# Optimization experiments

Hardware: AMD Instinct MI355X
Metric: run time of the kernel (lower is better)

The kernel has to match this reference:

```python
import jax, jax.numpy as jnp
import numpy as np

B, DIM, H, W = 64, 384, 28, 28
NH, HD, WS, SS = 6, 64, 7, 3
HID = 1536
N = WS * WS
NW = (H // WS) * (W // WS)
SCALE = HD ** -0.25  # qk_scale=None -> head_dim ** -0.25, applied to both q and k
EPS = 1e-5


def _rel_pos_index(ws):
    coords = np.stack(np.meshgrid(np.arange(ws), np.arange(ws), indexing='ij'))  # (2,ws,ws)
    flat = coords.reshape(2, -1)
    rel = (flat[:, :, None] - flat[:, None, :]).transpose(1, 2, 0).copy()  # (N,N,2)
    rel[..., 0] += ws - 1
    rel[..., 1] += ws - 1
    rel[..., 0] *= 2 * ws - 1
    return rel.sum(-1)  # (N,N) int


def _attn_mask(h, w, ws, ss):
    img = np.zeros((h, w))
    cnt = 0
    for hs in (slice(0, -ws), slice(-ws, -ss), slice(-ss, None)):
        for wsl in (slice(0, -ws), slice(-ws, -ss), slice(-ss, None)):
            img[hs, wsl] = cnt
            cnt += 1
    mw = img.reshape(h // ws, ws, w // ws, ws).transpose(0, 2, 1, 3).reshape(-1, ws * ws)  # (nW,N)
    diff = mw[:, None, :] - mw[:, :, None]
    return np.where(diff != 0, -100.0, 0.0).astype(np.float32)  # (nW,N,N)


REL_IDX = jnp.asarray(_rel_pos_index(WS))          # (N,N)
MASK = jnp.asarray(_attn_mask(H, W, WS, SS))       # (NW,N,N)


def _layernorm_bchw(x, w, b):
    mean = jnp.mean(x, axis=1, keepdims=True)
    var = jnp.var(x, axis=1, keepdims=True, ddof=1)  # torch.var_mean is unbiased
    return (x - mean) / jnp.sqrt(var + EPS) * w + b


def setup_inputs() -> dict:
    key = jax.random.key(0)
    ks = jax.random.split(key, 6)
    return {
        'x': jax.random.normal(ks[0], (B, DIM, H, W), jnp.float32),
        'norm1_w': jnp.ones((1, DIM, 1, 1), jnp.float32),
        'norm1_b': jnp.zeros((1, DIM, 1, 1), jnp.float32),
        'qkv_w': jax.random.normal(ks[1], (3 * NH * HD, DIM), jnp.float32) * 0.02,
        'rel_bias_table': jax.random.normal(ks[2], ((2 * WS - 1) ** 2, NH), jnp.float32) * 0.02,
        'proj_w': jax.random.normal(ks[3], (DIM, NH * HD), jnp.float32) * 0.02,
        'norm2_w': jnp.ones((1, DIM, 1, 1), jnp.float32),
        'norm2_b': jnp.zeros((1, DIM, 1, 1), jnp.float32),
        'mlp_w1': jax.random.normal(ks[4], (HID, DIM), jnp.float32) * 0.02,
        'mlp_w3': jax.random.normal(ks[5], (DIM, HID), jnp.float32) * 0.02,
    }


def reference(x, norm1_w, norm1_b, qkv_w, rel_bias_table, proj_w, norm2_w, norm2_b, mlp_w1, mlp_w3):
    b = x.shape[0]
    shortcut = x
    xn = _layernorm_bchw(x, norm1_w, norm1_b)
    xs = jnp.roll(xn, (-SS, -SS), axis=(2, 3))
    # window partition: (B,C,H,W) -> (B*nW, C, WS, WS)
    xw = xs.reshape(b, DIM, H // WS, WS, W // WS, WS).transpose(0, 2, 4, 1, 3, 5).reshape(-1, DIM, WS, WS)
    bw = xw.shape[0]
    # 1x1-conv qkv projection (no bias), then split heads
    qkv = jnp.einsum('oc,bchw->bohw', qkv_w, xw).reshape(bw, 3, NH, HD, N)
    q, k, v = jnp.moveaxis(qkv, 1, 0)  # each (bw, NH, HD, N)
    attn = jnp.einsum('bhdn,bhdm->bhnm', q * SCALE, k * SCALE)  # (bw,NH,N,N)
    bias = rel_bias_table[REL_IDX.reshape(-1)].reshape(N, N, NH).transpose(2, 0, 1)  # (NH,N,N)
    attn = attn + bias[None]
    attn = attn.reshape(b, NW, NH, N, N) + MASK[None, :, None]
    attn = jax.nn.softmax(attn.reshape(bw, NH, N, N), axis=-1)
    out = jnp.einsum('bhnm,bhdm->bhdn', attn, v)  # (bw,NH,HD,N)
    out = out.reshape(bw, NH * HD, WS, WS)
    out = jnp.einsum('oc,bchw->bohw', proj_w, out)
    # window reverse + unshift
    xr = out.reshape(b, H // WS, W // WS, DIM, WS, WS).transpose(0, 3, 1, 4, 2, 5).reshape(b, DIM, H, W)
    xr = jnp.roll(xr, (SS, SS), axis=(2, 3))
    x = shortcut + xr
    # conv MLP (1x1 convs, no bias, exact GELU)
    xn2 = _layernorm_bchw(x, norm2_w, norm2_b)
    h = jax.nn.gelu(jnp.einsum('oc,bchw->bohw', mlp_w1, xn2), approximate=False)
    x = x + jnp.einsum('oc,bchw->bohw', mlp_w3, h)
    return x
```

## Files before the change

kernel.cpp:

```cpp
#include <hip/hip_runtime.h>
#include <hip/hip_bf16.h>


typedef __bf16 bf16x8 __attribute__((ext_vector_type(8)));
typedef __bf16 bf16x4 __attribute__((ext_vector_type(4)));
typedef float  f32x4  __attribute__((ext_vector_type(4)));

#define GAS __attribute__((address_space(1)))
#define LAS __attribute__((address_space(3)))

__device__ __forceinline__ void gload_lds16(const void* g, void* l) {
  __builtin_amdgcn_global_load_lds((const GAS void*)g, (LAS void*)l, 16, 0, 0);
}

__device__ __forceinline__ int div7u(int m) { return (m * 37) >> 8; }

__device__ __forceinline__ float gelu_f(float v) {
  float s = fabsf(v) * 0.70710678118f;
  float t = __builtin_amdgcn_rcpf(__builtin_fmaf(0.3275911f, s, 1.f));
  float p = t * (0.254829592f +
            t * (-0.284496736f +
            t * (1.421413741f +
            t * (-1.453152027f +
            t * 1.061405429f))));
  float erfa = __builtin_fmaf(-p, __expf(-s * s), 1.f);
  return __builtin_fmaf(0.5f * fabsf(v), erfa, 0.5f * v);
}

__global__ __launch_bounds__(256) void cvt_all_kernel(const float* __restrict__ s0,
                                                      const float* __restrict__ s1,
                                                      const float* __restrict__ s2,
                                                      const float* __restrict__ s3,
                                                      __bf16* __restrict__ d0,
                                                      __bf16* __restrict__ d1,
                                                      __bf16* __restrict__ d2,
                                                      __bf16* __restrict__ d3) {
  int i = blockIdx.x * 256 + threadIdx.x;
  if (i < 442368) { d0[i] = (__bf16)s0[i]; return; }
  i -= 442368;
  if (i < 147456) { d1[i] = (__bf16)s1[i]; return; }
  i -= 147456;
  if (i < 589824) { d2[i] = (__bf16)s2[i]; return; }
  i -= 589824;
  d3[i] = (__bf16)s3[i];
}

__global__ __launch_bounds__(256) void bias_expand_kernel(const float* __restrict__ tbl,
                                                          float* __restrict__ be) {
  int idx = blockIdx.x * 256 + threadIdx.x;
  if (idx >= 6 * 64 * 64) return;
  int m = idx & 63, n = (idx >> 6) & 63, h = idx >> 12;
  float v = 0.f;
  if (m < 49 && n < 49) {
    int in_ = div7u(n), jn = n - in_ * 7;
    int im  = div7u(m), jm = m - im * 7;
    int t = (in_ - im + 6) * 13 + (jn - jm + 6);
    v = tbl[t * 6 + h];
  }
  be[idx] = v;
}

__global__ __launch_bounds__(256) void ln_t_kernel(const float* __restrict__ x,
                                                   const float* __restrict__ gw,
                                                   const float* __restrict__ gb,
                                                   __bf16* __restrict__ out) {
  __shared__ f32x4 ps[16][16], ps2[16][16];
  __shared__ __align__(16) __bf16 tile[64][198];
  const int tid = threadIdx.x;
  const int lane = tid & 63, w = tid >> 6;
  const int gq = lane & 15;
  const int sub = (w << 2) + (lane >> 4);
  const int tok0 = blockIdx.x << 6;
  const int tokg4 = tok0 + (gq << 2);
  const unsigned b = (unsigned)tokg4 / 784u;
  const unsigned p = (unsigned)tokg4 - b * 784u;
  const float* xp = x + (size_t)b * 301056u + p;

  f32x4 vals[24];
  f32x4 s4 = {0.f, 0.f, 0.f, 0.f}, s24 = {0.f, 0.f, 0.f, 0.f};
  #pragma unroll
  for (int half = 0; half < 2; ++half)
    #pragma unroll
    for (int k = 0; k < 12; ++k) {
      int c = half * 192 + sub * 12 + k;
      f32x4 v = *(const f32x4*)(xp + (size_t)c * 784u);
      vals[half * 12 + k] = v;
      s4 += v;
      s24 += v * v;
    }
  ps[sub][gq] = s4;
  ps2[sub][gq] = s24;
  __syncthreads();
  f32x4 S = {0.f, 0.f, 0.f, 0.f}, S2 = {0.f, 0.f, 0.f, 0.f};
  #pragma unroll
  for (int i = 0; i < 16; ++i) { S += ps[i][gq]; S2 += ps2[i][gq]; }
  f32x4 mean = S * (1.f / 384.f);
  f32x4 var = (S2 - S * mean) * (1.f / 383.f);
  f32x4 rstd;
  #pragma unroll
  for (int j = 0; j < 4; ++j) rstd[j] = rsqrtf(var[j] + 1e-5f);

  #pragma unroll
  for (int half = 0; half < 2; ++half) {
    if (half) __syncthreads();
    #pragma unroll
    for (int k = 0; k < 12; ++k) {
      int c = half * 192 + sub * 12 + k;
      float wgt = gw[c], bia = gb[c];
      f32x4 v = (vals[half * 12 + k] - mean) * rstd * wgt + bia;
      #pragma unroll
      for (int j = 0; j < 4; ++j)
        tile[(gq << 2) + j][sub * 12 + k] = (__bf16)v[j];
    }
    __syncthreads();
    #pragma unroll
    for (int it = 0; it < 6; ++it) {
      int idx = (it << 8) + tid;
      int row = idx / 24, colc = idx - row * 24;
      bf16x8 vv = *(const bf16x8*)(&tile[row][colc << 3]);
      *(bf16x8*)(out + (size_t)(tok0 + row) * 384 + half * 192 + (colc << 3)) = vv;
    }
  }
}

template <int EPI>
__global__ __launch_bounds__(256, 2) void gemm_bt(const __bf16* __restrict__ A, int lda,
                                                  const __bf16* __restrict__ Bt, int ldb,
                                                  int K, int My,
                                                  __bf16* __restrict__ outT, int ldo, int ocol,
                                                  float* __restrict__ outR,
                                                  const float* __restrict__ resid,
                                                  int tok_off) {
  __shared__ __align__(16) char smem[65536];
  const int tid = threadIdx.x;
  const int lane = tid & 63;
  const int w = tid >> 6;
  const int wr = w >> 1, wc = w & 1;
  const int c = lane & 15, g = lane >> 4;

  const int nwg = gridDim.x;
  const int orig = blockIdx.x;
  const int q = nwg >> 3, r = nwg & 7;
  const int xcd = orig & 7, ii = orig >> 3;
  const int base = xcd < r ? xcd * (q + 1) : r * (q + 1) + (xcd - r) * q;
  const int wgid = base + ii;
  const int bx = wgid / My;
  const int by = wgid - bx * My;
  const int m0 = by << 7;
  const int n0 = bx << 7;

  const __bf16* ap[4];
  const __bf16* bp[4];
  #pragma unroll
  for (int i = 0; i < 4; ++i) {
    int s = (i << 8) + tid;
    int row = s >> 3;
    int kk = ((s ^ row) & 7) << 3;
    ap[i] = A  + (size_t)(m0 + row) * lda + kk;
    bp[i] = Bt + (size_t)(n0 + row) * ldb + kk;
  }
  auto stage = [&](int buf, int k0) {
    #pragma unroll
    for (int i = 0; i < 4; ++i) {
      gload_lds16(ap[i] + k0, smem + (buf << 15) + (((i << 8) + (w << 6)) << 4));
      gload_lds16(bp[i] + k0, smem + (buf << 15) + 16384 + (((i << 8) + (w << 6)) << 4));
    }
  };

  f32x4 acc[4][4] = {};
  const int nt = K >> 6;
  stage(0, 0);
  int cur = 0;
  for (int t = 0; t < nt; ++t) {
    if (t + 1 < nt) {
      stage(cur ^ 1, (t + 1) << 6);
      asm volatile("s_waitcnt vmcnt(8)" ::: "memory");
    } else {
      asm volatile("s_waitcnt vmcnt(0)" ::: "memory");
    }
    __builtin_amdgcn_s_barrier();
    __builtin_amdgcn_sched_barrier(0);
    const char* smA = smem + (cur << 15);
    const char* smB = smA + 16384;
    #pragma unroll
    for (int ks = 0; ks < 2; ++ks) {
      bf16x8 af[4], bfv[4];
      #pragma unroll
      for (int mi = 0; mi < 4; ++mi) {
        int r2 = (wr << 6) + (mi << 4) + c;
        af[mi] = *(const bf16x8*)(smA + (r2 << 7) + (((ks << 6) + (g << 4)) ^ ((r2 & 7) << 4)));
      }
      #pragma unroll
      for (int nj = 0; nj < 4; ++nj) {
        int r2 = (wc << 6) + (nj << 4) + c;
        bfv[nj] = *(const bf16x8*)(smB + (r2 << 7) + (((ks << 6) + (g << 4)) ^ ((r2 & 7) << 4)));
      }
      #pragma unroll
      for (int mi = 0; mi < 4; ++mi)
        #pragma unroll
        for (int nj = 0; nj < 4; ++nj) {
          if constexpr (EPI == 2)
            acc[mi][nj] = __builtin_amdgcn_mfma_f32_16x16x32_bf16(bfv[nj], af[mi], acc[mi][nj], 0, 0, 0);
          else
            acc[mi][nj] = __builtin_amdgcn_mfma_f32_16x16x32_bf16(af[mi], bfv[nj], acc[mi][nj], 0, 0, 0);
        }
    }
    __builtin_amdgcn_s_barrier();
    cur ^= 1;
  }

  if constexpr (EPI <= 1) {
    #pragma unroll
    for (int mi = 0; mi < 4; ++mi)
      #pragma unroll
      for (int nj = 0; nj < 4; ++nj) {
        f32x4 v = acc[mi][nj];
        if constexpr (EPI == 1) {
          #pragma unroll
          for (int r2 = 0; r2 < 4; ++r2) v[r2] = gelu_f(v[r2]);
        }
        bf16x4 pk = {(__bf16)v[0], (__bf16)v[1], (__bf16)v[2], (__bf16)v[3]};
        int nl = (wc << 6) + (nj << 4) + c;
        int ml = (wr << 6) + (mi << 4) + (g << 2);
        *(bf16x4*)(smem + nl * 264 + ml * 2) = pk;
      }
    __syncthreads();
    #pragma unroll
    for (int it = 0; it < 8; ++it) {
      int id = (it << 8) + tid;
      int n = id >> 4, mc = id & 15;
      bf16x8 v = *(const bf16x8*)(smem + n * 264 + (mc << 4));
      *(bf16x8*)(outT + (size_t)(n0 + n) * ldo + (ocol + m0 + (mc << 3))) = v;
    }
  } else {
    #pragma unroll
    for (int nj = 0; nj < 4; ++nj) {
      int tokb = tok_off + n0 + (wc << 6) + (nj << 4) + (g << 2);
      unsigned bb = (unsigned)tokb / 784u;
      unsigned pp = (unsigned)tokb - bb * 784u;
      size_t base2 = (size_t)bb * (384u * 784u) + pp;
      #pragma unroll
      for (int mi = 0; mi < 4; ++mi) {
        int o = m0 + (wr << 6) + (mi << 4) + c;
        size_t a2 = base2 + (size_t)o * 784u;
        f32x4 rv = *(const f32x4*)(resid + a2);
        f32x4 v = acc[mi][nj] + rv;
        *(f32x4*)(outR + a2) = v;
      }
    }
  }
}

__global__ __launch_bounds__(256, 2) void attn_kernel(const __bf16* __restrict__ qkv,
                                                      const float* __restrict__ be,
                                                      __bf16* __restrict__ outt) {
  __shared__ __align__(16) char smem_all[4][16384];
  const int tid = threadIdx.x;
  const int lane = tid & 63;
  const int w = tid >> 6;
  char* sm = (char*)smem_all[w];
  const int pair = blockIdx.x * 4 + w;
  const int h = pair % 6;
  const int wg = pair / 6;
  const int b = wg >> 4;
  const int wi = wg & 15;
  const int wh = wi >> 2, wwi = wi & 3;
  const int cc = lane & 15, g = lane >> 4;

  {
    int rsub = lane >> 3;
    int slot = lane & 7;
    int dc = (slot ^ rsub) << 3;
    #pragma unroll
    for (int i = 0; i < 8; ++i) {
      int r = i * 8 + rsub;
      int m = r < 49 ? r : 48;
      int im = div7u(m), jm = m - im * 7;
      int sh = wh * 7 + im + 3; if (sh >= 28) sh -= 28;
      int sw = wwi * 7 + jm + 3; if (sw >= 28) sw -= 28;
      size_t trow = (size_t)(b * 784 + sh * 28 + sw) * 1152;
      gload_lds16(qkv + trow + 384 + h * 64 + dc, sm + i * 1024);
      gload_lds16(qkv + trow +       h * 64 + dc, sm + 8192 + i * 1024);
    }
  }
  asm volatile("s_waitcnt vmcnt(0)" ::: "memory");
  __syncthreads();

  f32x4 sacc[4][4] = {};
  #pragma unroll
  for (int ks = 0; ks < 2; ++ks) {
    bf16x8 kf[4], qf[4];
    #pragma unroll
    for (int mi = 0; mi < 4; ++mi) {
      int r = (mi << 4) + cc;
      kf[mi] = *(const bf16x8*)(sm + (r << 7) + (((ks << 6) + (g << 4)) ^ ((r & 7) << 4)));
    }
    #pragma unroll
    for (int nj = 0; nj < 4; ++nj) {
      int r = (nj << 4) + cc;
      qf[nj] = *(const bf16x8*)(sm + 8192 + (r << 7) + (((ks << 6) + (g << 4)) ^ ((r & 7) << 4)));
    }
    #pragma unroll
    for (int mi = 0; mi < 4; ++mi)
      #pragma unroll
      for (int nj = 0; nj < 4; ++nj)
        sacc[mi][nj] = __builtin_amdgcn_mfma_f32_16x16x32_bf16(kf[mi], qf[nj], sacc[mi][nj], 0, 0, 0);
  }
  __syncthreads();

  int r9m[4][4];
  #pragma unroll
  for (int mi = 0; mi < 4; ++mi)
    #pragma unroll
    for (int rr = 0; rr < 4; ++rr) {
      int m = (mi << 4) + (g << 2) + rr; if (m > 48) m = 48;
      int im = div7u(m), jm = m - im * 7;
      int sh = wh * 7 + im, sw = wwi * 7 + jm;
      r9m[mi][rr] = ((sh < 21) ? 0 : (sh < 25 ? 1 : 2)) * 3 + ((sw < 21) ? 0 : (sw < 25 ? 1 : 2));
    }

  #pragma unroll
  for (int nj = 0; nj < 4; ++nj) {
    int n = (nj << 4) + cc;
    int ncl = n > 48 ? 48 : n;
    int in_ = div7u(ncl), jn = ncl - in_ * 7;
    int shn = wh * 7 + in_, swn = wwi * 7 + jn;
    int r9n = ((shn < 21) ? 0 : (shn < 25 ? 1 : 2)) * 3 + ((swn < 21) ? 0 : (swn < 25 ? 1 : 2));
    float mx = -1e30f;
    #pragma unroll
    for (int mi = 0; mi < 4; ++mi) {
      f32x4 bia = *(const f32x4*)(be + (((h << 6) + n) << 6) + (mi << 4) + (g << 2));
      #pragma unroll
      for (int rr = 0; rr < 4; ++rr) {
        int m = (mi << 4) + (g << 2) + rr;
        float t = (m < 49)
            ? sacc[mi][nj][rr] * 0.125f + bia[rr] + ((r9m[mi][rr] == r9n) ? 0.f : -100.f)
            : -1e30f;
        sacc[mi][nj][rr] = t;
        mx = fmaxf(mx, t);
      }
    }
    mx = fmaxf(mx, __shfl_xor(mx, 16, 64));
    mx = fmaxf(mx, __shfl_xor(mx, 32, 64));
    float sum = 0.f;
    #pragma unroll
    for (int mi = 0; mi < 4; ++mi)
      #pragma unroll
      for (int rr = 0; rr < 4; ++rr) {
        float e = __expf(sacc[mi][nj][rr] - mx);
        sacc[mi][nj][rr] = e;
        sum += e;
      }
    sum += __shfl_xor(sum, 16, 64);
    sum += __shfl_xor(sum, 32, 64);
    float inv = __builtin_amdgcn_rcpf(sum);
    #pragma unroll
    for (int mi = 0; mi < 4; ++mi) {
      bf16x4 pk = {(__bf16)(sacc[mi][nj][0] * inv), (__bf16)(sacc[mi][nj][1] * inv),
                   (__bf16)(sacc[mi][nj][2] * inv), (__bf16)(sacc[mi][nj][3] * inv)};
      *(bf16x4*)(sm + 8192 + (n << 7) + (((mi << 5) + (g << 3)) ^ ((n & 7) << 4))) = pk;
    }
  }

  {
    int ml = lane & 15, dq = lane >> 4;
    #pragma unroll
    for (int it = 0; it < 4; ++it) {
      int m = (it << 4) + ml;
      int mc_ = m > 48 ? 48 : m;
      int im = div7u(mc_), jm = mc_ - im * 7;
      int sh = wh * 7 + im + 3; if (sh >= 28) sh -= 28;
      int sw = wwi * 7 + jm + 3; if (sw >= 28) sw -= 28;
      const __bf16* gv = qkv + (size_t)(b * 784 + sh * 28 + sw) * 1152 + 768 + h * 64;
      #pragma unroll
      for (int hd = 0; hd < 2; ++hd) {
        int dbase = (hd << 5) + (dq << 3);
        bf16x8 v = *(const bf16x8*)(gv + dbase);
        #pragma unroll
        for (int j = 0; j < 8; ++j) {
          int d = dbase + j;
          *(__bf16*)(sm + (d << 7) + ((((m >> 3) ^ (d & 7)) << 4) + ((m & 7) << 1))) = v[j];
        }
      }
    }
  }
  __syncthreads();

  f32x4 oacc[4][4] = {};
  #pragma unroll
  for (int ks = 0; ks < 2; ++ks) {
    bf16x8 pf[4], vf[4];
    #pragma unroll
    for (int ni = 0; ni < 4; ++ni) {
      int n = (ni << 4) + cc;
      pf[ni] = *(const bf16x8*)(sm + 8192 + (n << 7) + (((ks << 6) + (g << 4)) ^ ((n & 7) << 4)));
    }
    #pragma unroll
    for (int dj = 0; dj < 4; ++dj) {
      int d = (dj << 4) + cc;
      vf[dj] = *(const bf16x8*)(sm + (d << 7) + ((((ks << 2) + g) ^ (d & 7)) << 4));
    }
    #pragma unroll
    for (int ni = 0; ni < 4; ++ni)
      #pragma unroll
      for (int dj = 0; dj < 4; ++dj)
        oacc[ni][dj] = __builtin_amdgcn_mfma_f32_16x16x32_bf16(pf[ni], vf[dj], oacc[ni][dj], 0, 0, 0);
  }

  #pragma unroll
  for (int ni = 0; ni < 4; ++ni)
    #pragma unroll
    for (int rr = 0; rr < 4; ++rr) {
      int n = (ni << 4) + (g << 2) + rr;
      if (n < 49) {
        int im = div7u(n), jn = n - im * 7;
        int sh = wh * 7 + im + 3; if (sh >= 28) sh -= 28;
        int sw = wwi * 7 + jn + 3; if (sw >= 28) sw -= 28;
        __bf16* op = outt + (size_t)(b * 784 + sh * 28 + sw) * 384 + h * 64;
        #pragma unroll
        for (int dj = 0; dj < 4; ++dj)
          op[(dj << 4) + cc] = (__bf16)oacc[ni][dj][rr];
      }
    }
}

extern "C" void kernel_launch(void* const* d_in, const int* in_sizes, int n_in,
                              void* d_out, int out_size, void* d_ws, size_t ws_size,
                              hipStream_t stream) {
  (void)in_sizes; (void)n_in; (void)out_size; (void)ws_size;
  const float* x     = (const float*)d_in[0];
  const float* n1w   = (const float*)d_in[1];
  const float* n1b   = (const float*)d_in[2];
  const float* qkvw  = (const float*)d_in[3];
  const float* tbl   = (const float*)d_in[4];
  const float* projw = (const float*)d_in[5];
  const float* n2w   = (const float*)d_in[6];
  const float* n2b   = (const float*)d_in[7];
  const float* w1    = (const float*)d_in[8];
  const float* w3    = (const float*)d_in[9];
  float* out = (float*)d_out;

  char* ws = (char*)d_ws;
  __bf16* bufA = (__bf16*)ws;
  __bf16* bufB = (__bf16*)(ws + 38535168);
  float*  be   = (float*)(ws + 154140672);
  __bf16* wq   = (__bf16*)(ws + 154238976);
  __bf16* wp   = wq + 442368;
  __bf16* wm1  = wp + 147456;
  __bf16* wm3  = wm1 + 589824;

  cvt_all_kernel<<<6912, 256, 0, stream>>>(qkvw, projw, w1, w3, wq, wp, wm1, wm3);
  bias_expand_kernel<<<96, 256, 0, stream>>>(tbl, be);

  ln_t_kernel<<<784, 256, 0, stream>>>(x, n1w, n1b, bufA);
  gemm_bt<0><<<392 * 9, 256, 0, stream>>>(wq, 384, bufA, 384, 384, 9, bufB, 1152, 0,
                                          nullptr, nullptr, 0);
  attn_kernel<<<1536, 256, 0, stream>>>(bufB, be, bufA);
  gemm_bt<2><<<392 * 3, 256, 0, stream>>>(wp, 384, bufA, 384, 384, 3, nullptr, 0, 0,
                                          out, x, 0);
  ln_t_kernel<<<784, 256, 0, stream>>>(out, n2w, n2b, bufA);
  for (int hh = 0; hh < 2; ++hh) {
    const int toff = hh * 25088;
    gemm_bt<1><<<196 * 12, 256, 0, stream>>>(wm1, 384, bufA + (size_t)toff * 384, 384, 384, 12,
                                             bufB, 1536, 0, nullptr, nullptr, 0);
    gemm_bt<2><<<196 * 3, 256, 0, stream>>>(wm3, 1536, bufB, 1536, 1536, 3,
                                            nullptr, 0, 0, out, out, toff);
  }
}
```

Before: 399.1 us.

## Add 256x256-tile 8-wave GEMM for QKV and MLP-up projections

Adds a new gemm256 kernel with 256x256 output tiles, 512 threads, K fixed at 384, staged double buffering interleaved with MFMA phases and s_setprio hints. It replaces the 128x128 gemm_bt for the QKV projection (M padded from 1152 to 1280 with clamped loads and a masked store) and the MLP first layer with GELU. The larger tile raises arithmetic intensity and cuts global and LDS traffic per FLOP. In exchange it uses 128KB of LDS and many accumulator registers, which limits occupancy, and wastes compute on the padded M rows for QKV. gemm_bt is reduced to the residual-add epilogue only.

```diff
diff --git a/kernel.cpp b/kernel.cpp
--- a/kernel.cpp
+++ b/kernel.cpp
@@ -124,10 +124,160 @@
 }
 
 template <int EPI>
+__global__ __launch_bounds__(512, 2) void gemm256(const __bf16* __restrict__ A,
+                                                  const __bf16* __restrict__ Bt, int ldb,
+                                                  int My, int Mreal,
+                                                  __bf16* __restrict__ outT, int ldo) {
+  __shared__ __align__(16) char smem[131072];
+  const int tid = threadIdx.x;
+  const int lane = tid & 63;
+  const int w = tid >> 6;
+  const int wr = w >> 2, wc = w & 3;
+  const int c = lane & 15, g = lane >> 4;
+
+  const int nwg = gridDim.x;
+  const int orig = blockIdx.x;
+  const int q = nwg >> 3, r = nwg & 7;
+  const int xcd = orig & 7, ii = orig >> 3;
+  const int wgid = (xcd < r ? xcd * (q + 1) : r * (q + 1) + (xcd - r) * q) + ii;
+  const int bx = wgid / My;
+  const int by = wgid - bx * My;
+  const int m0 = by << 8;
+  const int n0 = bx << 8;
+
+  const int r0 = tid >> 3;
+  const int kk = ((tid & 7) ^ ((tid >> 3) & 7)) << 3;
+  const __bf16* pA[4];
+  const __bf16* pB[4];
+  #pragma unroll
+  for (int j = 0; j < 4; ++j) {
+    int ra = m0 + j * 64 + r0; if (ra > Mreal - 1) ra = Mreal - 1;
+    pA[j] = A + (size_t)ra * 384 + kk;
+    pB[j] = Bt + (size_t)(n0 + j * 64 + r0) * ldb + kk;
+  }
+  const int dstw = w << 10;
+  auto stage = [&](int buf, int ht, int k0) {
+    char* d = smem + (buf << 16) + (ht << 14) + dstw;
+    const __bf16* p0 = (ht < 2) ? pA[ht << 1] : pB[(ht - 2) << 1];
+    const __bf16* p1 = (ht < 2) ? pA[(ht << 1) + 1] : pB[((ht - 2) << 1) + 1];
+    gload_lds16(p0 + k0, d);
+    gload_lds16(p1 + k0, d + 8192);
+  };
+
+  const int off0 = (g << 4) ^ ((c & 7) << 4);
+  const int off1 = off0 ^ 64;
+  const int aB = (wr << 14) + (c << 7);
+  const int bB = 32768 + (wc << 13) + (c << 7);
+
+  f32x4 acc[8][4];
+  #pragma unroll
+  for (int i = 0; i < 8; ++i)
+    #pragma unroll
+    for (int j = 0; j < 4; ++j) acc[i][j] = (f32x4){0.f, 0.f, 0.f, 0.f};
+
+  stage(0, 0, 0); stage(0, 1, 0); stage(0, 2, 0); stage(0, 3, 0);
+
+  bf16x8 aX[4], aY[4], b0[4], b1[4];
+  #pragma unroll
+  for (int t = 0; t < 6; ++t) {
+    const int cur = t & 1, nxt = cur ^ 1;
+    const int k1 = (t + 1) << 6;
+    const char* sc = smem + (cur << 16);
+    __builtin_amdgcn_s_barrier();
+    if (t < 5) {
+      stage(nxt, 0, k1);
+      asm volatile("s_waitcnt vmcnt(2)" ::: "memory");
+    } else {
+      asm volatile("s_waitcnt vmcnt(0)" ::: "memory");
+    }
+    __builtin_amdgcn_s_barrier();
+    #pragma unroll
+    for (int mi = 0; mi < 4; ++mi) aX[mi] = *(const bf16x8*)(sc + aB + mi * 2048 + off0);
+    #pragma unroll
+    for (int nj = 0; nj < 4; ++nj) b0[nj] = *(const bf16x8*)(sc + bB + nj * 2048 + off0);
+    asm volatile("s_waitcnt lgkmcnt(0)" ::: "memory");
+    __builtin_amdgcn_sched_barrier(0);
+    __builtin_amdgcn_s_setprio(1);
+    #pragma unroll
+    for (int mi = 0; mi < 4; ++mi)
+      #pragma unroll
+      for (int nj = 0; nj < 4; ++nj)
+        acc[mi][nj] = __builtin_amdgcn_mfma_f32_16x16x32_bf16(aX[mi], b0[nj], acc[mi][nj], 0, 0, 0);
+    __builtin_amdgcn_s_setprio(0);
+    #pragma unroll
+    for (int mi = 0; mi < 4; ++mi) aY[mi] = *(const bf16x8*)(sc + aB + (4 + mi) * 2048 + off0);
+    if (t < 5) stage(nxt, 1, k1);
+    asm volatile("s_waitcnt lgkmcnt(0)" ::: "memory");
+    __builtin_amdgcn_sched_barrier(0);
+    __builtin_amdgcn_s_setprio(1);
+    #pragma unroll
+    for (int mi = 0; mi < 4; ++mi)
+      #pragma unroll
+      for (int nj = 0; nj < 4; ++nj)
+        acc[4 + mi][nj] = __builtin_amdgcn_mfma_f32_16x16x32_bf16(aY[mi], b0[nj], acc[4 + mi][nj], 0, 0, 0);
+    __builtin_amdgcn_s_setprio(0);
+    #pragma unroll
+    for (int mi = 0; mi < 4; ++mi) aX[mi] = *(const bf16x8*)(sc + aB + mi * 2048 + off1);
+    #pragma unroll
+    for (int nj = 0; nj < 4; ++nj) b1[nj] = *(const bf16x8*)(sc + bB + nj * 2048 + off1);
+    if (t < 5) stage(nxt, 2, k1);
+    asm volatile("s_waitcnt lgkmcnt(0)" ::: "memory");
+    __builtin_amdgcn_sched_barrier(0);
+    __builtin_amdgcn_s_setprio(1);
+    #pragma unroll
+    for (int mi = 0; mi < 4; ++mi)
+      #pragma unroll
+      for (int nj = 0; nj < 4; ++nj)
+        acc[mi][nj] = __builtin_amdgcn_mfma_f32_16x16x32_bf16(aX[mi], b1[nj], acc[mi][nj], 0, 0, 0);
+    __builtin_amdgcn_s_setprio(0);
+    #pragma unroll
+    for (int mi = 0; mi < 4; ++mi) aY[mi] = *(const bf16x8*)(sc + aB + (4 + mi) * 2048 + off1);
+    if (t < 5) stage(nxt, 3, k1);
+    asm volatile("s_waitcnt lgkmcnt(0)" ::: "memory");
+    __builtin_amdgcn_sched_barrier(0);
+    __builtin_amdgcn_s_setprio(1);
+    #pragma unroll
+    for (int mi = 0; mi < 4; ++mi)
+      #pragma unroll
+      for (int nj = 0; nj < 4; ++nj)
+        acc[4 + mi][nj] = __builtin_amdgcn_mfma_f32_16x16x32_bf16(aY[mi], b1[nj], acc[4 + mi][nj], 0, 0, 0);
+    __builtin_amdgcn_s_setprio(0);
+  }
+
+  __syncthreads();
+  char* tw = smem + (w << 14);
+  #pragma unroll
+  for (int mi = 0; mi < 8; ++mi)
+    #pragma unroll
+    for (int nj = 0; nj < 4; ++nj) {
+      f32x4 v = acc[mi][nj];
+      if constexpr (EPI == 1) {
+        #pragma unroll
+        for (int j = 0; j < 4; ++j) v[j] = gelu_f(v[j]);
+      }
+      bf16x4 pk = {(__bf16)v[0], (__bf16)v[1], (__bf16)v[2], (__bf16)v[3]};
+      int tok = (nj << 4) + c;
+      int mb = (mi << 5) + (g << 3);
+      *(bf16x4*)(tw + (tok << 8) + (mb ^ ((tok & 7) << 4))) = pk;
+    }
+  __syncthreads();
+  const int tokl = lane >> 4;
+  const int ch = lane & 15;
+  const int mg = m0 + (wr << 7) + (ch << 3);
+  if (mg < Mreal) {
+    #pragma unroll
+    for (int rep = 0; rep < 16; ++rep) {
+      int tok = (rep << 2) + tokl;
+      bf16x8 v = *(const bf16x8*)(tw + (tok << 8) + ((ch << 4) ^ ((tok & 7) << 4)));
+      *(bf16x8*)(outT + (size_t)(n0 + (wc << 6) + tok) * ldo + mg) = v;
+    }
+  }
+}
+
+template <int EPI>
 __global__ __launch_bounds__(256, 2) void gemm_bt(const __bf16* __restrict__ A, int lda,
                                                   const __bf16* __restrict__ Bt, int ldb,
                                                   int K, int My,
-                                                  __bf16* __restrict__ outT, int ldo, int ocol,
                                                   float* __restrict__ outR,
                                                   const float* __restrict__ resid,
                                                   int tok_off) {
@@ -155,9 +305,9 @@
   for (int i = 0; i < 4; ++i) {
     int s = (i << 8) + tid;
     int row = s >> 3;
-    int kk = ((s ^ row) & 7) << 3;
-    ap[i] = A  + (size_t)(m0 + row) * lda + kk;
-    bp[i] = Bt + (size_t)(n0 + row) * ldb + kk;
+    int kkk = ((s ^ row) & 7) << 3;
+    ap[i] = A  + (size_t)(m0 + row) * lda + kkk;
+    bp[i] = Bt + (size_t)(n0 + row) * ldb + kkk;
   }
   auto stage = [&](int buf, int k0) {
     #pragma unroll
@@ -198,55 +348,26 @@
       #pragma unroll
       for (int mi = 0; mi < 4; ++mi)
         #pragma unroll
-        for (int nj = 0; nj < 4; ++nj) {
-          if constexpr (EPI == 2)
-            acc[mi][nj] = __builtin_amdgcn_mfma_f32_16x16x32_bf16(bfv[nj], af[mi], acc[mi][nj], 0, 0, 0);
-          else
-            acc[mi][nj] = __builtin_amdgcn_mfma_f32_16x16x32_bf16(af[mi], bfv[nj], acc[mi][nj], 0, 0, 0);
-        }
+        for (int nj = 0; nj < 4; ++nj)
+          acc[mi][nj] = __builtin_amdgcn_mfma_f32_16x16x32_bf16(bfv[nj], af[mi], acc[mi][nj], 0, 0, 0);
     }
     __builtin_amdgcn_s_barrier();
     cur ^= 1;
   }
 
-  if constexpr (EPI <= 1) {
-    #pragma unroll
-    for (int mi = 0; mi < 4; ++mi)
-      #pragma unroll
-      for (int nj = 0; nj < 4; ++nj) {
-        f32x4 v = acc[mi][nj];
-        if constexpr (EPI == 1) {
-          #pragma unroll
-          for (int r2 = 0; r2 < 4; ++r2) v[r2] = gelu_f(v[r2]);
-        }
-        bf16x4 pk = {(__bf16)v[0], (__bf16)v[1], (__bf16)v[2], (__bf16)v[3]};
-        int nl = (wc << 6) + (nj << 4) + c;
-        int ml = (wr << 6) + (mi << 4) + (g << 2);
-        *(bf16x4*)(smem + nl * 264 + ml * 2) = pk;
-      }
-    __syncthreads();
-    #pragma unroll
-    for (int it = 0; it < 8; ++it) {
-      int id = (it << 8) + tid;
-      int n = id >> 4, mc = id & 15;
-      bf16x8 v = *(const bf16x8*)(smem + n * 264 + (mc << 4));
-      *(bf16x8*)(outT + (size_t)(n0 + n) * ldo + (ocol + m0 + (mc << 3))) = v;
-    }
-  } else {
-    #pragma unroll
-    for (int nj = 0; nj < 4; ++nj) {
-      int tokb = tok_off + n0 + (wc << 6) + (nj << 4) + (g << 2);
-      unsigned bb = (unsigned)tokb / 784u;
-      unsigned pp = (unsigned)tokb - bb * 784u;
-      size_t base2 = (size_t)bb * (384u * 784u) + pp;
-      #pragma unroll
-      for (int mi = 0; mi < 4; ++mi) {
-        int o = m0 + (wr << 6) + (mi << 4) + c;
-        size_t a2 = base2 + (size_t)o * 784u;
-        f32x4 rv = *(const f32x4*)(resid + a2);
-        f32x4 v = acc[mi][nj] + rv;
-        *(f32x4*)(outR + a2) = v;
-      }
+  #pragma unroll
+  for (int nj = 0; nj < 4; ++nj) {
+    int tokb = tok_off + n0 + (wc << 6) + (nj << 4) + (g << 2);
+    unsigned bb = (unsigned)tokb / 784u;
+    unsigned pp = (unsigned)tokb - bb * 784u;
+    size_t base2 = (size_t)bb * (384u * 784u) + pp;
+    #pragma unroll
+    for (int mi = 0; mi < 4; ++mi) {
+      int o = m0 + (wr << 6) + (mi << 4) + c;
+      size_t a2 = base2 + (size_t)o * 784u;
+      f32x4 rv = *(const f32x4*)(resid + a2);
+      f32x4 v = acc[mi][nj] + rv;
+      *(f32x4*)(outR + a2) = v;
     }
   }
 }
@@ -453,17 +574,15 @@
   bias_expand_kernel<<<96, 256, 0, stream>>>(tbl, be);
 
   ln_t_kernel<<<784, 256, 0, stream>>>(x, n1w, n1b, bufA);
-  gemm_bt<0><<<392 * 9, 256, 0, stream>>>(wq, 384, bufA, 384, 384, 9, bufB, 1152, 0,
-                                          nullptr, nullptr, 0);
+  gemm256<0><<<196 * 5, 512, 0, stream>>>(wq, bufA, 384, 5, 1152, bufB, 1152);
   attn_kernel<<<1536, 256, 0, stream>>>(bufB, be, bufA);
-  gemm_bt<2><<<392 * 3, 256, 0, stream>>>(wp, 384, bufA, 384, 384, 3, nullptr, 0, 0,
-                                          out, x, 0);
+  gemm_bt<2><<<392 * 3, 256, 0, stream>>>(wp, 384, bufA, 384, 384, 3, out, x, 0);
   ln_t_kernel<<<784, 256, 0, stream>>>(out, n2w, n2b, bufA);
   for (int hh = 0; hh < 2; ++hh) {
     const int toff = hh * 25088;
-    gemm_bt<1><<<196 * 12, 256, 0, stream>>>(wm1, 384, bufA + (size_t)toff * 384, 384, 384, 12,
-                                             bufB, 1536, 0, nullptr, nullptr, 0);
+    gemm256<1><<<98 * 6, 512, 0, stream>>>(wm1, bufA + (size_t)toff * 384, 384, 6, 1536,
+                                           bufB, 1536);
     gemm_bt<2><<<196 * 3, 256, 0, stream>>>(wm3, 1536, bufB, 1536, 1536, 3,
-                                            nullptr, 0, 0, out, out, toff);
-  }
-}
+                                            out, out, toff);
+  }
+}
```

Result: slower. 419.6 us (+5.1%).

## Replace double-buffered direct-to-LDS GEMM loads with register-staged single buffer

Applied to the files above, without the earlier changes.

The GEMM kernel stops using global_load_lds into two LDS buffers. It now prefetches the next K tile into registers during the MFMA loop and writes it to a single LDS buffer between two barriers. This halves LDS use, which allows launch bounds of three workgroups per CU for higher occupancy. In exchange it adds VGPR pressure, register-to-LDS store traffic and an extra barrier per iteration, and the global load latency is only hidden within a single compute phase.

```diff
diff --git a/kernel.cpp b/kernel.cpp
--- a/kernel.cpp
+++ b/kernel.cpp
@@ -5,13 +5,10 @@
 typedef __bf16 bf16x8 __attribute__((ext_vector_type(8)));
 typedef __bf16 bf16x4 __attribute__((ext_vector_type(4)));
 typedef float  f32x4  __attribute__((ext_vector_type(4)));
+typedef int    i32x4  __attribute__((ext_vector_type(4)));
 
 #define GAS __attribute__((address_space(1)))
 #define LAS __attribute__((address_space(3)))
-
-__device__ __forceinline__ void gload_lds16(const void* g, void* l) {
-  __builtin_amdgcn_global_load_lds((const GAS void*)g, (LAS void*)l, 16, 0, 0);
-}
 
 __device__ __forceinline__ int div7u(int m) { return (m * 37) >> 8; }
 
@@ -124,14 +121,14 @@
 }
 
 template <int EPI>
-__global__ __launch_bounds__(256, 2) void gemm_bt(const __bf16* __restrict__ A, int lda,
+__global__ __launch_bounds__(256, 3) void gemm_bt(const __bf16* __restrict__ A, int lda,
                                                   const __bf16* __restrict__ Bt, int ldb,
                                                   int K, int My,
                                                   __bf16* __restrict__ outT, int ldo, int ocol,
                                                   float* __restrict__ outR,
                                                   const float* __restrict__ resid,
                                                   int tok_off) {
-  __shared__ __align__(16) char smem[65536];
+  __shared__ __align__(16) char smem[33792];
   const int tid = threadIdx.x;
   const int lane = tid & 63;
   const int w = tid >> 6;
@@ -142,8 +139,7 @@
   const int orig = blockIdx.x;
   const int q = nwg >> 3, r = nwg & 7;
   const int xcd = orig & 7, ii = orig >> 3;
-  const int base = xcd < r ? xcd * (q + 1) : r * (q + 1) + (xcd - r) * q;
-  const int wgid = base + ii;
+  const int wgid = (xcd < r ? xcd * (q + 1) : r * (q + 1) + (xcd - r) * q) + ii;
   const int bx = wgid / My;
   const int by = wgid - bx * My;
   const int m0 = by << 7;
@@ -159,29 +155,38 @@
     ap[i] = A  + (size_t)(m0 + row) * lda + kk;
     bp[i] = Bt + (size_t)(n0 + row) * ldb + kk;
   }
-  auto stage = [&](int buf, int k0) {
-    #pragma unroll
-    for (int i = 0; i < 4; ++i) {
-      gload_lds16(ap[i] + k0, smem + (buf << 15) + (((i << 8) + (w << 6)) << 4));
-      gload_lds16(bp[i] + k0, smem + (buf << 15) + 16384 + (((i << 8) + (w << 6)) << 4));
-    }
+
+  i32x4 sA0, sA1, sA2, sA3, sB0, sB1, sB2, sB3;
+  auto issue = [&](int k0) {
+    sA0 = *(const i32x4*)(ap[0] + k0); sB0 = *(const i32x4*)(bp[0] + k0);
+    sA1 = *(const i32x4*)(ap[1] + k0); sB1 = *(const i32x4*)(bp[1] + k0);
+    sA2 = *(const i32x4*)(ap[2] + k0); sB2 = *(const i32x4*)(bp[2] + k0);
+    sA3 = *(const i32x4*)(ap[3] + k0); sB3 = *(const i32x4*)(bp[3] + k0);
+  };
+  auto write_lds = [&]() {
+    *(i32x4*)(smem +         (((0 << 8) + tid) << 4)) = sA0;
+    *(i32x4*)(smem +         (((1 << 8) + tid) << 4)) = sA1;
+    *(i32x4*)(smem +         (((2 << 8) + tid) << 4)) = sA2;
+    *(i32x4*)(smem +         (((3 << 8) + tid) << 4)) = sA3;
+    *(i32x4*)(smem + 16384 + (((0 << 8) + tid) << 4)) = sB0;
+    *(i32x4*)(smem + 16384 + (((1 << 8) + tid) << 4)) = sB1;
+    *(i32x4*)(smem + 16384 + (((2 << 8) + tid) << 4)) = sB2;
+    *(i32x4*)(smem + 16384 + (((3 << 8) + tid) << 4)) = sB3;
   };
 
   f32x4 acc[4][4] = {};
   const int nt = K >> 6;
-  stage(0, 0);
-  int cur = 0;
+
+  issue(0);
+  write_lds();
+  asm volatile("s_waitcnt lgkmcnt(0)" ::: "memory");
+  __builtin_amdgcn_s_barrier();
+  __builtin_amdgcn_sched_barrier(0);
+
   for (int t = 0; t < nt; ++t) {
-    if (t + 1 < nt) {
-      stage(cur ^ 1, (t + 1) << 6);
-      asm volatile("s_waitcnt vmcnt(8)" ::: "memory");
-    } else {
-      asm volatile("s_waitcnt vmcnt(0)" ::: "memory");
-    }
-    __builtin_amdgcn_s_barrier();
-    __builtin_amdgcn_sched_barrier(0);
-    const char* smA = smem + (cur << 15);
-    const char* smB = smA + 16384;
+    if (t + 1 < nt) issue((t + 1) << 6);
+    const char* smA = smem;
+    const char* smB = smem + 16384;
     #pragma unroll
     for (int ks = 0; ks < 2; ++ks) {
       bf16x8 af[4], bfv[4];
@@ -206,7 +211,12 @@
         }
     }
     __builtin_amdgcn_s_barrier();
-    cur ^= 1;
+    if (t + 1 < nt) {
+      write_lds();
+      asm volatile("s_waitcnt lgkmcnt(0)" ::: "memory");
+    }
+    __builtin_amdgcn_s_barrier();
+    __builtin_amdgcn_sched_barrier(0);
   }
 
   if constexpr (EPI <= 1) {
@@ -279,8 +289,10 @@
       int sh = wh * 7 + im + 3; if (sh >= 28) sh -= 28;
       int sw = wwi * 7 + jm + 3; if (sw >= 28) sw -= 28;
       size_t trow = (size_t)(b * 784 + sh * 28 + sw) * 1152;
-      gload_lds16(qkv + trow + 384 + h * 64 + dc, sm + i * 1024);
-      gload_lds16(qkv + trow +       h * 64 + dc, sm + 8192 + i * 1024);
+      __builtin_amdgcn_global_load_lds((const GAS void*)(qkv + trow + 384 + h * 64 + dc),
+                                       (LAS void*)(sm + i * 1024), 16, 0, 0);
+      __builtin_amdgcn_global_load_lds((const GAS void*)(qkv + trow + h * 64 + dc),
+                                       (LAS void*)(sm + 8192 + i * 1024), 16, 0, 0);
     }
   }
   asm volatile("s_waitcnt vmcnt(0)" ::: "memory");
```

Result: no change. 401.1 us (+0.5%).
